# Performance work log

Hardware: AMD Instinct MI355X
Metric: run time of the kernel (lower is better)

## Reference

```python
import jax, jax.numpy as jnp
import numpy as np

HIDDEN = 2048
HEADS = 16
HEAD_DIM = HIDDEN // HEADS
BLOCK = 64
SEQ = 4096
NUM_BLOCKS = SEQ // BLOCK
N_LOCAL = 3
N_GLOBAL = 1
N_RANDOM = 1
SCALE = 1.0 / np.sqrt(HEAD_DIM)


def _sparse_mask(rand_idx):
    # rand_idx: [num_blocks, n_random] int -- random key-block per query-block row
    i = jnp.arange(NUM_BLOCKS)[:, None]
    j = jnp.arange(NUM_BLOCKS)[None, :]
    half = N_LOCAL // 2
    local = (j >= i - half) & (j <= i + half)
    glob = (j < N_GLOBAL) | (j >= NUM_BLOCKS - N_GLOBAL)
    rand = jnp.any(j[:, :, None] == rand_idx[:, None, :], axis=-1)
    blk = local | glob | rand                      # [nb, nb] bool
    full = jnp.repeat(jnp.repeat(blk, BLOCK, axis=0), BLOCK, axis=1)
    return full[:SEQ, :SEQ]                        # [S, S] bool


def setup_inputs() -> dict:
    key = jax.random.key(0)
    k1, k2, k3, k4, k5, k6 = jax.random.split(key, 6)
    s = 0.02
    return {
        "hidden_states": jax.random.normal(k1, (1, SEQ, HIDDEN), jnp.float32),
        "rand_idx": jax.random.randint(k2, (NUM_BLOCKS, N_RANDOM), 0, NUM_BLOCKS, jnp.int32),
        "Wq": jax.random.normal(k3, (HIDDEN, HIDDEN), jnp.float32) * s,
        "Wk": jax.random.normal(k4, (HIDDEN, HIDDEN), jnp.float32) * s,
        "Wv": jax.random.normal(k5, (HIDDEN, HIDDEN), jnp.float32) * s,
        "Wo": jax.random.normal(k6, (HIDDEN, HIDDEN), jnp.float32) * s,
    }


def reference(hidden_states, rand_idx, Wq, Wk, Wv, Wo):
    B, S, _ = hidden_states.shape
    # torch Linear: y = x @ W.T
    q = (hidden_states @ Wq.T).reshape(B, S, HEADS, HEAD_DIM).transpose(0, 2, 1, 3)
    k = (hidden_states @ Wk.T).reshape(B, S, HEADS, HEAD_DIM).transpose(0, 2, 1, 3)
    v = (hidden_states @ Wv.T).reshape(B, S, HEADS, HEAD_DIM).transpose(0, 2, 1, 3)
    scores = jnp.einsum("bhqd,bhkd->bhqk", q, k) * SCALE
    mask = _sparse_mask(rand_idx)                  # [S, S] bool
    scores = jnp.where(mask[None, None, :, :], scores, -jnp.inf)
    probs = jax.nn.softmax(scores, axis=-1)
    out = jnp.einsum("bhqk,bhkd->bhqd", probs, v)
    out = out.transpose(0, 2, 1, 3).reshape(B, S, HIDDEN)
    return out @ Wo.T
```

## Files before the change

kernel.cpp:

```cpp
#include <hip/hip_runtime.h>

typedef unsigned short u16;
typedef unsigned short u16x8 __attribute__((ext_vector_type(8)));
typedef __bf16 bf16x8 __attribute__((ext_vector_type(8)));
typedef float f32x4 __attribute__((ext_vector_type(4)));

#define SEQQ 4096
#define HID 2048
#define HD 128
#define NBLK 64
#define ATT_SCALE 0.08838834764831843f

__device__ __forceinline__ u16 f2bf(float f) {
    unsigned u = __float_as_uint(f);
    u += 0x7fffu + ((u >> 16) & 1u);
    return (u16)(u >> 16);
}

__device__ __forceinline__ void gload_lds16(const void* g, void* l) {
    __builtin_amdgcn_global_load_lds((const __attribute__((address_space(1))) void*)g,
                                     (__attribute__((address_space(3))) void*)l, 16, 0, 0);
}

__global__ __launch_bounds__(256) void cvt_bf16_k(const float* __restrict__ in,
                                                  u16* __restrict__ out, int n4) {
    int i = blockIdx.x * 256 + threadIdx.x;
    if (i < n4) {
        float4 v = ((const float4*)in)[i];
        ushort4 o;
        o.x = f2bf(v.x); o.y = f2bf(v.y); o.z = f2bf(v.z); o.w = f2bf(v.w);
        ((ushort4*)out)[i] = o;
    }
}

__global__ __launch_bounds__(256) void cvt4_k(const float* __restrict__ w0,
                                              const float* __restrict__ w1,
                                              const float* __restrict__ w2,
                                              const float* __restrict__ w3,
                                              u16* __restrict__ qkv,
                                              u16* __restrict__ wo) {
    const int y = blockIdx.y;
    const float* src = (y == 0) ? w0 : (y == 1) ? w1 : (y == 2) ? w2 : w3;
    u16* dst = (y < 3) ? (qkv + (size_t)y * 4194304) : wo;
    int i = blockIdx.x * 256 + threadIdx.x;
    float4 v = ((const float4*)src)[i];
    ushort4 o;
    o.x = f2bf(v.x); o.y = f2bf(v.y); o.z = f2bf(v.z); o.w = f2bf(v.w);
    ((ushort4*)dst)[i] = o;
}

#define QUAD(MH, AF, BF)                                                        \
    __builtin_amdgcn_s_setprio(1);                                              \
    _Pragma("unroll") for (int mi = 0; mi < 4; ++mi) {                          \
        _Pragma("unroll") for (int ni = 0; ni < 4; ++ni)                        \
            acc[(MH) * 4 + mi][ni] = __builtin_amdgcn_mfma_f32_16x16x32_bf16(   \
                (AF)[mi], (BF)[ni], acc[(MH) * 4 + mi][ni], 0, 0, 0);           \
    }                                                                           \
    __builtin_amdgcn_s_setprio(0);

template <int MODE>
__global__ __launch_bounds__(512, 2) void gemm256(const u16* __restrict__ A,
                                                  const u16* __restrict__ B,
                                                  void* __restrict__ C0,
                                                  u16* __restrict__ C1,
                                                  u16* __restrict__ C2,
                                                  int M, int N, int K) {
    __shared__ __align__(16) u16 As[2][2][4][256][8];
    __shared__ __align__(16) u16 Bs[2][2][4][256][8];
    const int t = threadIdx.x, w = t >> 6, l = t & 63;
    const int wm = w >> 2, wn = w & 3, ll = l & 15, lg = l >> 4;

    const int gx = gridDim.x, gy = gridDim.y;
    const int nwg = gx * gy;
    int lid = blockIdx.y * gx + blockIdx.x;
    int swz = (lid & 7) * (nwg >> 3) + (lid >> 3);
    const int mb = swz % gy, nb = swz / gy;

    const int c1 = t, c2 = t + 512;
    const u16* gA1 = A + (size_t)(mb * 256 + (c1 & 255)) * K + (c1 >> 8) * 8;
    const u16* gA2 = A + (size_t)(mb * 256 + (c2 & 255)) * K + (c2 >> 8) * 8;
    const u16* gB1 = B + (size_t)(nb * 256 + (c1 & 255)) * K + (c1 >> 8) * 8;
    const u16* gB2 = B + (size_t)(nb * 256 + (c2 & 255)) * K + (c2 >> 8) * 8;

    f32x4 acc[8][4] = {};

    auto stageA = [&](int buf, int kh, int kt) {
        gload_lds16(gA1 + kt * 64 + kh * 32, &As[buf][kh][c1 >> 8][c1 & 255][0]);
        gload_lds16(gA2 + kt * 64 + kh * 32, &As[buf][kh][c2 >> 8][c2 & 255][0]);
    };
    auto stageB = [&](int buf, int kh, int kt) {
        gload_lds16(gB1 + kt * 64 + kh * 32, &Bs[buf][kh][c1 >> 8][c1 & 255][0]);
        gload_lds16(gB2 + kt * 64 + kh * 32, &Bs[buf][kh][c2 >> 8][c2 & 255][0]);
    };
    auto fragsA = [&](int buf, int kh, int mh, bf16x8* af) {
#pragma unroll
        for (int mi = 0; mi < 4; ++mi)
            af[mi] = *(const bf16x8*)&As[buf][kh][lg][wm * 128 + mh * 64 + mi * 16 + ll][0];
    };
    auto fragsB = [&](int buf, int kh, bf16x8* bf) {
#pragma unroll
        for (int ni = 0; ni < 4; ++ni)
            bf[ni] = *(const bf16x8*)&Bs[buf][kh][lg][wn * 64 + ni * 16 + ll][0];
    };

    stageA(0, 0, 0); stageB(0, 0, 0); stageA(0, 1, 0); stageB(0, 1, 0);
    asm volatile("s_waitcnt vmcnt(4)" ::: "memory");
    asm volatile("s_barrier" ::: "memory");

    const int T = K >> 6;
    for (int kt = 0; kt < T; ++kt) {
        const int buf = kt & 1, nbuf = buf ^ 1;
        const bool last = (kt == T - 1);
        bf16x8 a0[4], a1[4], b0[4];
        fragsA(buf, 0, 0, a0); fragsB(buf, 0, b0);
        if (!last) stageA(nbuf, 0, kt + 1);
        asm volatile("s_barrier" ::: "memory");
        QUAD(0, a0, b0)
        asm volatile("s_barrier" ::: "memory");
        fragsA(buf, 0, 1, a1);
        if (!last) {
            stageB(nbuf, 0, kt + 1);
            asm volatile("s_waitcnt vmcnt(4)" ::: "memory");
        } else {
            asm volatile("s_waitcnt vmcnt(0)" ::: "memory");
        }
        asm volatile("s_barrier" ::: "memory");
        QUAD(1, a1, b0)
        asm volatile("s_barrier" ::: "memory");
        fragsA(buf, 1, 0, a0); fragsB(buf, 1, b0);
        if (!last) stageA(nbuf, 1, kt + 1);
        asm volatile("s_barrier" ::: "memory");
        QUAD(0, a0, b0)
        asm volatile("s_barrier" ::: "memory");
        fragsA(buf, 1, 1, a1);
        if (!last) {
            stageB(nbuf, 1, kt + 1);
            asm volatile("s_waitcnt vmcnt(4)" ::: "memory");
        }
        asm volatile("s_barrier" ::: "memory");
        QUAD(1, a1, b0)
        asm volatile("s_barrier" ::: "memory");
    }

    const int colb = nb * 256;
    u16* dstq = nullptr;
    int coff = 0;
    if (MODE == 1) {
        if (colb < 2048)      { dstq = (u16*)C0; coff = colb; }
        else if (colb < 4096) { dstq = C1; coff = colb - 2048; }
        else                  { dstq = C2; coff = colb - 4096; }
    }
#pragma unroll
    for (int mi = 0; mi < 8; ++mi)
#pragma unroll
        for (int ni = 0; ni < 4; ++ni) {
            f32x4 v = acc[mi][ni];
#pragma unroll
            for (int r = 0; r < 4; ++r) {
                int row = mb * 256 + wm * 128 + mi * 16 + lg * 4 + r;
                int col = wn * 64 + ni * 16 + ll;
                if (MODE == 0)
                    ((float*)C0)[(size_t)row * N + colb + col] = v[r];
                else
                    dstq[(size_t)row * 2048 + coff + col] = f2bf(v[r]);
            }
        }
}

__global__ __launch_bounds__(256) void transpose_k(const u16* __restrict__ in,
                                                   u16* __restrict__ out) {
    __shared__ __align__(16) u16 tl[64][64];
    const int s0 = blockIdx.x * 64, d0 = blockIdx.y * 64;
    const int t = threadIdx.x;
#pragma unroll
    for (int j = 0; j < 2; ++j) {
        int c = j * 256 + t;
        int sr = c >> 3, c8 = c & 7;
        u16x8 v = *(const u16x8*)&in[(size_t)(s0 + sr) * 2048 + d0 + c8 * 8];
        *(u16x8*)&tl[sr][(c8 ^ (sr >> 3)) * 8] = v;
    }
    __syncthreads();
#pragma unroll
    for (int j = 0; j < 2; ++j) {
        int c = j * 256 + t;
        int dr = c >> 3, sg = c & 7;
        u16x8 v;
#pragma unroll
        for (int i = 0; i < 8; ++i)
            v[i] = tl[sg * 8 + i][(((dr >> 3) ^ sg) * 8) + (dr & 7)];
        *(u16x8*)&out[(size_t)(d0 + dr) * 4096 + s0 + sg * 8] = v;
    }
}

__global__ __launch_bounds__(256) void sparse_attn(const u16* __restrict__ Q,
                                                   const u16* __restrict__ Kmat,
                                                   const u16* __restrict__ Vt,
                                                   const int* __restrict__ rnd,
                                                   u16* __restrict__ Out) {
    __shared__ __align__(16) u16 Ks[2][8192];
    __shared__ __align__(16) u16 Vs[2][8192];
    __shared__ __align__(16) char Plds[4 * 2048];

    const int qb = blockIdx.x, h = blockIdx.y;
    const int t = threadIdx.x, w = t >> 6, l = t & 63;
    const int lg = l >> 4, ll = l & 15;

    int blist[6];
    int nblk = 0;
    {
        int cands[6];
        cands[0] = qb - 1; cands[1] = qb; cands[2] = qb + 1;
        cands[3] = 0; cands[4] = NBLK - 1; cands[5] = rnd[qb];
        for (int c = 0; c < 6; ++c) {
            int b = cands[c];
            if (b < 0 || b >= NBLK) continue;
            bool dup = false;
            for (int j = 0; j < nblk; ++j) dup = dup || (blist[j] == b);
            if (!dup) blist[nblk++] = b;
        }
    }

    auto stage = [&](int buf, int kb) {
        const u16* kbase = Kmat + (size_t)(kb * 64) * HID + h * HD;
        const u16* vbase = Vt + (size_t)(h * HD) * SEQQ + kb * 64;
#pragma unroll
        for (int j = 0; j < 4; ++j) {
            int d = j * 256 + t;
            int kr = d >> 4, kc_ = (d & 15) ^ (kr & 7);
            gload_lds16(kbase + (size_t)kr * HID + kc_ * 8, &Ks[buf][d * 8]);
            int vr = d >> 3, vc = (d & 7) ^ (vr & 7);
            gload_lds16(vbase + (size_t)vr * SEQQ + vc * 8, &Vs[buf][d * 8]);
        }
    };

    bf16x8 qf[4];
    const int qrow = qb * 64 + w * 16 + ll;
#pragma unroll
    for (int kc = 0; kc < 4; ++kc)
        qf[kc] = *(const bf16x8*)&Q[(size_t)qrow * HID + h * HD + kc * 32 + lg * 8];

    f32x4 o[8];
#pragma unroll
    for (int dt = 0; dt < 8; ++dt) o[dt] = (f32x4){0.f, 0.f, 0.f, 0.f};
    float mrun[4], lrun[4];
#pragma unroll
    for (int r = 0; r < 4; ++r) { mrun[r] = -1e30f; lrun[r] = 0.f; }

    char* Pw = Plds + w * 2048;

    stage(0, blist[0]);
    int cur = 0;

    for (int bi = 0; bi < nblk; ++bi) {
        if (bi + 1 < nblk) {
            stage(cur ^ 1, blist[bi + 1]);
            asm volatile("s_waitcnt vmcnt(8)\n\ts_barrier" ::: "memory");
        } else {
            asm volatile("s_waitcnt vmcnt(0)\n\ts_barrier" ::: "memory");
        }

        f32x4 s[4];
#pragma unroll
        for (int ct = 0; ct < 4; ++ct) s[ct] = (f32x4){0.f, 0.f, 0.f, 0.f};
#pragma unroll
        for (int ct = 0; ct < 4; ++ct) {
            const int krow = ct * 16 + ll;
#pragma unroll
            for (int kc = 0; kc < 4; ++kc) {
                bf16x8 kf = *(const bf16x8*)&Ks[cur][krow * 128 +
                                                    (((kc * 4 + lg) ^ (krow & 7)) << 3)];
                s[ct] = __builtin_amdgcn_mfma_f32_16x16x32_bf16(qf[kc], kf, s[ct], 0, 0, 0);
            }
        }

        float rmax[4];
#pragma unroll
        for (int r = 0; r < 4; ++r) {
            s[0][r] *= ATT_SCALE; s[1][r] *= ATT_SCALE;
            s[2][r] *= ATT_SCALE; s[3][r] *= ATT_SCALE;
            rmax[r] = fmaxf(fmaxf(s[0][r], s[1][r]), fmaxf(s[2][r], s[3][r]));
        }
#pragma unroll
        for (int mk = 1; mk <= 8; mk <<= 1)
#pragma unroll
            for (int r = 0; r < 4; ++r)
                rmax[r] = fmaxf(rmax[r], __shfl_xor(rmax[r], mk));

        float scl[4], psum[4];
#pragma unroll
        for (int r = 0; r < 4; ++r) {
            float mn = fmaxf(mrun[r], rmax[r]);
            scl[r] = __expf(mrun[r] - mn);
            mrun[r] = mn;
            psum[r] = 0.f;
        }

#pragma unroll
        for (int ct = 0; ct < 4; ++ct)
#pragma unroll
            for (int r = 0; r < 4; ++r) {
                float e = __expf(s[ct][r] - mrun[r]);
                psum[r] += e;
                const int q = lg * 4 + r;
                const int kv = ct * 16 + ll;
                *(u16*)(Pw + q * 128 + ((kv * 2) ^ ((q & 7) << 4))) = f2bf(e);
            }
#pragma unroll
        for (int mk = 1; mk <= 8; mk <<= 1)
#pragma unroll
            for (int r = 0; r < 4; ++r)
                psum[r] += __shfl_xor(psum[r], mk);
#pragma unroll
        for (int r = 0; r < 4; ++r)
            lrun[r] = lrun[r] * scl[r] + psum[r];
#pragma unroll
        for (int dt = 0; dt < 8; ++dt)
#pragma unroll
            for (int r = 0; r < 4; ++r)
                o[dt][r] *= scl[r];

#pragma unroll
        for (int kc2 = 0; kc2 < 2; ++kc2) {
            bf16x8 pf = *(const bf16x8*)(Pw + ll * 128 +
                                         ((kc2 * 64 + lg * 16) ^ ((ll & 7) << 4)));
#pragma unroll
            for (int dt = 0; dt < 8; ++dt) {
                const int vrow = dt * 16 + ll;
                bf16x8 vf = *(const bf16x8*)&Vs[cur][vrow * 64 +
                                                     (((kc2 * 4 + lg) ^ (vrow & 7)) << 3)];
                o[dt] = __builtin_amdgcn_mfma_f32_16x16x32_bf16(pf, vf, o[dt], 0, 0, 0);
            }
        }

        asm volatile("s_barrier" ::: "memory");
        cur ^= 1;
    }

    float rl[4];
#pragma unroll
    for (int r = 0; r < 4; ++r) rl[r] = 1.f / lrun[r];
#pragma unroll
    for (int dt = 0; dt < 8; ++dt)
#pragma unroll
        for (int r = 0; r < 4; ++r) {
            int row = qb * 64 + w * 16 + lg * 4 + r;
            int col = h * HD + dt * 16 + ll;
            Out[(size_t)row * HID + col] = f2bf(o[dt][r] * rl[r]);
        }
}

extern "C" void kernel_launch(void* const* d_in, const int* in_sizes, int n_in,
                              void* d_out, int out_size, void* d_ws, size_t ws_size,
                              hipStream_t stream) {
    const float* hs = (const float*)d_in[0];
    const int* rnd = (const int*)d_in[1];
    const float* Wq = (const float*)d_in[2];
    const float* Wk = (const float*)d_in[3];
    const float* Wv = (const float*)d_in[4];
    const float* Wo = (const float*)d_in[5];
    float* out = (float*)d_out;

    char* ws = (char*)d_ws;
    u16* hs_b   = (u16*)(ws);
    u16* Wqkv_b = (u16*)(ws + 16777216);
    u16* Wo_b   = (u16*)(ws + 41943040);
    u16* Qb     = (u16*)(ws + 50331648);
    u16* Kb     = (u16*)(ws + 67108864);
    u16* Vtb    = (u16*)(ws + 83886080);
    u16* Ab     = (u16*)(ws + 100663296);

    cvt_bf16_k<<<dim3(8192), 256, 0, stream>>>(hs, hs_b, 8388608 / 4);
    cvt4_k<<<dim3(4096, 4), 256, 0, stream>>>(Wq, Wk, Wv, Wo, Wqkv_b, Wo_b);

    gemm256<1><<<dim3(24, 16), 512, 0, stream>>>(hs_b, Wqkv_b, Qb, Kb, Ab, 4096, 6144, 2048);

    transpose_k<<<dim3(64, 32), 256, 0, stream>>>(Ab, Vtb);

    sparse_attn<<<dim3(64, 16), 256, 0, stream>>>(Qb, Kb, Vtb, rnd, Ab);

    gemm256<0><<<dim3(8, 16), 512, 0, stream>>>(Ab, Wo_b, out, nullptr, nullptr, 4096, 2048, 2048);
}
```

Baseline: 477.0 us.

## Use 128x256 GEMM tiles with triple-buffered LDS and load attention V directly

```diff
diff --git a/kernel.cpp b/kernel.cpp
--- a/kernel.cpp
+++ b/kernel.cpp
@@ -49,97 +49,95 @@
     ((ushort4*)dst)[i] = o;
 }
 
-#define QUAD(MH, AF, BF)                                                        \
-    __builtin_amdgcn_s_setprio(1);                                              \
-    _Pragma("unroll") for (int mi = 0; mi < 4; ++mi) {                          \
-        _Pragma("unroll") for (int ni = 0; ni < 4; ++ni)                        \
-            acc[(MH) * 4 + mi][ni] = __builtin_amdgcn_mfma_f32_16x16x32_bf16(   \
-                (AF)[mi], (BF)[ni], acc[(MH) * 4 + mi][ni], 0, 0, 0);           \
-    }                                                                           \
-    __builtin_amdgcn_s_setprio(0);
-
 template <int MODE>
-__global__ __launch_bounds__(512, 2) void gemm256(const u16* __restrict__ A,
-                                                  const u16* __restrict__ B,
-                                                  void* __restrict__ C0,
-                                                  u16* __restrict__ C1,
-                                                  u16* __restrict__ C2,
-                                                  int M, int N, int K) {
-    __shared__ __align__(16) u16 As[2][2][4][256][8];
-    __shared__ __align__(16) u16 Bs[2][2][4][256][8];
+__global__ __launch_bounds__(512, 2) void gemm_p(const u16* __restrict__ A,
+                                                 const u16* __restrict__ B,
+                                                 void* __restrict__ C0,
+                                                 u16* __restrict__ C1,
+                                                 u16* __restrict__ C2,
+                                                 int M, int N, int K) {
+    __shared__ __align__(16) u16 As[3][2][4][128][8];
+    __shared__ __align__(16) u16 Bs[3][2][4][256][8];
     const int t = threadIdx.x, w = t >> 6, l = t & 63;
-    const int wm = w >> 2, wn = w & 3, ll = l & 15, lg = l >> 4;
+    const int ll = l & 15, lg = l >> 4;
+    const int wm = w >> 2, wn = w & 3;
 
     const int gx = gridDim.x, gy = gridDim.y;
-    const int nwg = gx * gy;
+    const int per = (gx * gy) >> 3;
     int lid = blockIdx.y * gx + blockIdx.x;
-    int swz = (lid & 7) * (nwg >> 3) + (lid >> 3);
-    const int mb = swz % gy, nb = swz / gy;
-
-    const int c1 = t, c2 = t + 512;
-    const u16* gA1 = A + (size_t)(mb * 256 + (c1 & 255)) * K + (c1 >> 8) * 8;
-    const u16* gA2 = A + (size_t)(mb * 256 + (c2 & 255)) * K + (c2 >> 8) * 8;
-    const u16* gB1 = B + (size_t)(nb * 256 + (c1 & 255)) * K + (c1 >> 8) * 8;
-    const u16* gB2 = B + (size_t)(nb * 256 + (c2 & 255)) * K + (c2 >> 8) * 8;
-
-    f32x4 acc[8][4] = {};
-
-    auto stageA = [&](int buf, int kh, int kt) {
-        gload_lds16(gA1 + kt * 64 + kh * 32, &As[buf][kh][c1 >> 8][c1 & 255][0]);
-        gload_lds16(gA2 + kt * 64 + kh * 32, &As[buf][kh][c2 >> 8][c2 & 255][0]);
+    int virt = (lid & 7) * per + (lid >> 3);
+    const int nb = virt % gx, mb = virt / gx;
+
+    f32x4 acc[4][4] = {};
+
+    const int akg = (t >> 7) & 3, arow = t & 127;
+    const int bkg = t >> 8, brow = t & 255;
+    const u16* gA = A + (size_t)(mb * 128 + arow) * K + akg * 8;
+    const u16* gB = B + (size_t)(nb * 256 + brow) * K;
+
+    auto stageA = [&](int sb, int kt) {
+        const u16* p = gA + kt * 64;
+        gload_lds16(p, &As[sb][0][akg][arow][0]);
+        gload_lds16(p + 32, &As[sb][1][akg][arow][0]);
     };
-    auto stageB = [&](int buf, int kh, int kt) {
-        gload_lds16(gB1 + kt * 64 + kh * 32, &Bs[buf][kh][c1 >> 8][c1 & 255][0]);
-        gload_lds16(gB2 + kt * 64 + kh * 32, &Bs[buf][kh][c2 >> 8][c2 & 255][0]);
+    auto stageB = [&](int sb, int kt) {
+        const u16* p = gB + kt * 64;
+        gload_lds16(p + bkg * 8,        &Bs[sb][0][bkg][brow][0]);
+        gload_lds16(p + (bkg + 2) * 8,  &Bs[sb][0][bkg + 2][brow][0]);
+        gload_lds16(p + 32 + bkg * 8,   &Bs[sb][1][bkg][brow][0]);
+        gload_lds16(p + 32 + (bkg + 2) * 8, &Bs[sb][1][bkg + 2][brow][0]);
     };
-    auto fragsA = [&](int buf, int kh, int mh, bf16x8* af) {
+
+    stageA(0, 0); stageB(0, 0); stageA(1, 1); stageB(1, 1);
+    asm volatile("s_waitcnt vmcnt(6)" ::: "memory");
+    __builtin_amdgcn_s_barrier();
+
+    const int T = K >> 6;
+    int buf = 0;
+    for (int kt = 0; kt < T; ++kt) {
+        const int sb = (buf + 2 >= 3) ? buf - 1 : buf + 2;
+        const bool st = (kt + 2) < T;
+        bf16x8 af[4], bfr[4];
 #pragma unroll
         for (int mi = 0; mi < 4; ++mi)
-            af[mi] = *(const bf16x8*)&As[buf][kh][lg][wm * 128 + mh * 64 + mi * 16 + ll][0];
-    };
-    auto fragsB = [&](int buf, int kh, bf16x8* bf) {
+            af[mi] = *(const bf16x8*)&As[buf][0][lg][wm * 64 + mi * 16 + ll][0];
 #pragma unroll
         for (int ni = 0; ni < 4; ++ni)
-            bf[ni] = *(const bf16x8*)&Bs[buf][kh][lg][wn * 64 + ni * 16 + ll][0];
-    };
-
-    stageA(0, 0, 0); stageB(0, 0, 0); stageA(0, 1, 0); stageB(0, 1, 0);
-    asm volatile("s_waitcnt vmcnt(4)" ::: "memory");
-    asm volatile("s_barrier" ::: "memory");
-
-    const int T = K >> 6;
-    for (int kt = 0; kt < T; ++kt) {
-        const int buf = kt & 1, nbuf = buf ^ 1;
-        const bool last = (kt == T - 1);
-        bf16x8 a0[4], a1[4], b0[4];
-        fragsA(buf, 0, 0, a0); fragsB(buf, 0, b0);
-        if (!last) stageA(nbuf, 0, kt + 1);
-        asm volatile("s_barrier" ::: "memory");
-        QUAD(0, a0, b0)
-        asm volatile("s_barrier" ::: "memory");
-        fragsA(buf, 0, 1, a1);
-        if (!last) {
-            stageB(nbuf, 0, kt + 1);
-            asm volatile("s_waitcnt vmcnt(4)" ::: "memory");
+            bfr[ni] = *(const bf16x8*)&Bs[buf][0][lg][wn * 64 + ni * 16 + ll][0];
+        if (st) stageA(sb, kt + 2);
+        __builtin_amdgcn_s_barrier();
+        __builtin_amdgcn_s_setprio(1);
+#pragma unroll
+        for (int mi = 0; mi < 4; ++mi)
+#pragma unroll
+            for (int ni = 0; ni < 4; ++ni)
+                acc[mi][ni] = __builtin_amdgcn_mfma_f32_16x16x32_bf16(af[mi], bfr[ni],
+                                                                      acc[mi][ni], 0, 0, 0);
+        __builtin_amdgcn_s_setprio(0);
+        bf16x8 ag[4], bgr[4];
+#pragma unroll
+        for (int mi = 0; mi < 4; ++mi)
+            ag[mi] = *(const bf16x8*)&As[buf][1][lg][wm * 64 + mi * 16 + ll][0];
+#pragma unroll
+        for (int ni = 0; ni < 4; ++ni)
+            bgr[ni] = *(const bf16x8*)&Bs[buf][1][lg][wn * 64 + ni * 16 + ll][0];
+        if (st) {
+            stageB(sb, kt + 2);
+            asm volatile("s_waitcnt vmcnt(6)" ::: "memory");
         } else {
             asm volatile("s_waitcnt vmcnt(0)" ::: "memory");
         }
-        asm volatile("s_barrier" ::: "memory");
-        QUAD(1, a1, b0)
-        asm volatile("s_barrier" ::: "memory");
-        fragsA(buf, 1, 0, a0); fragsB(buf, 1, b0);
-        if (!last) stageA(nbuf, 1, kt + 1);
-        asm volatile("s_barrier" ::: "memory");
-        QUAD(0, a0, b0)
-        asm volatile("s_barrier" ::: "memory");
-        fragsA(buf, 1, 1, a1);
-        if (!last) {
-            stageB(nbuf, 1, kt + 1);
-            asm volatile("s_waitcnt vmcnt(4)" ::: "memory");
-        }
-        asm volatile("s_barrier" ::: "memory");
-        QUAD(1, a1, b0)
-        asm volatile("s_barrier" ::: "memory");
+        __builtin_amdgcn_s_barrier();
+        __builtin_amdgcn_s_setprio(1);
+#pragma unroll
+        for (int mi = 0; mi < 4; ++mi)
+#pragma unroll
+            for (int ni = 0; ni < 4; ++ni)
+                acc[mi][ni] = __builtin_amdgcn_mfma_f32_16x16x32_bf16(ag[mi], bgr[ni],
+                                                                      acc[mi][ni], 0, 0, 0);
+        __builtin_amdgcn_s_setprio(0);
+        __builtin_amdgcn_s_barrier();
+        buf = (buf + 1 == 3) ? 0 : buf + 1;
     }
 
     const int colb = nb * 256;
@@ -151,13 +149,13 @@
         else                  { dstq = C2; coff = colb - 4096; }
     }
 #pragma unroll
-    for (int mi = 0; mi < 8; ++mi)
+    for (int mi = 0; mi < 4; ++mi)
 #pragma unroll
         for (int ni = 0; ni < 4; ++ni) {
             f32x4 v = acc[mi][ni];
 #pragma unroll
             for (int r = 0; r < 4; ++r) {
-                int row = mb * 256 + wm * 128 + mi * 16 + lg * 4 + r;
+                int row = mb * 128 + wm * 64 + mi * 16 + lg * 4 + r;
                 int col = wn * 64 + ni * 16 + ll;
                 if (MODE == 0)
                     ((float*)C0)[(size_t)row * N + colb + col] = v[r];
@@ -197,8 +195,7 @@
                                                    const u16* __restrict__ Vt,
                                                    const int* __restrict__ rnd,
                                                    u16* __restrict__ Out) {
-    __shared__ __align__(16) u16 Ks[2][8192];
-    __shared__ __align__(16) u16 Vs[2][8192];
+    __shared__ __align__(16) u16 Ks[3][8192];
     __shared__ __align__(16) char Plds[4 * 2048];
 
     const int qb = blockIdx.x, h = blockIdx.y;
@@ -220,16 +217,13 @@
         }
     }
 
-    auto stage = [&](int buf, int kb) {
+    auto stageK = [&](int sb, int kb) {
         const u16* kbase = Kmat + (size_t)(kb * 64) * HID + h * HD;
-        const u16* vbase = Vt + (size_t)(h * HD) * SEQQ + kb * 64;
 #pragma unroll
         for (int j = 0; j < 4; ++j) {
             int d = j * 256 + t;
             int kr = d >> 4, kc_ = (d & 15) ^ (kr & 7);
-            gload_lds16(kbase + (size_t)kr * HID + kc_ * 8, &Ks[buf][d * 8]);
-            int vr = d >> 3, vc = (d & 7) ^ (vr & 7);
-            gload_lds16(vbase + (size_t)vr * SEQQ + vc * 8, &Vs[buf][d * 8]);
+            gload_lds16(kbase + (size_t)kr * HID + kc_ * 8, &Ks[sb][d * 8]);
         }
     };
 
@@ -248,16 +242,31 @@
 
     char* Pw = Plds + w * 2048;
 
-    stage(0, blist[0]);
-    int cur = 0;
+    stageK(0, blist[0]);
+    if (nblk > 1) stageK(1, blist[1]);
+    int buf = 0;
 
     for (int bi = 0; bi < nblk; ++bi) {
-        if (bi + 1 < nblk) {
-            stage(cur ^ 1, blist[bi + 1]);
-            asm volatile("s_waitcnt vmcnt(8)\n\ts_barrier" ::: "memory");
+        const int kb = blist[bi];
+        const bool st = (bi + 2) < nblk;
+        const int sb = (buf + 2 >= 3) ? buf - 1 : buf + 2;
+        if (st) {
+            stageK(sb, blist[bi + 2]);
+            asm volatile("s_waitcnt vmcnt(8)" ::: "memory");
+        } else if (bi + 1 < nblk) {
+            asm volatile("s_waitcnt vmcnt(4)" ::: "memory");
         } else {
-            asm volatile("s_waitcnt vmcnt(0)\n\ts_barrier" ::: "memory");
-        }
+            asm volatile("s_waitcnt vmcnt(0)" ::: "memory");
+        }
+        __builtin_amdgcn_s_barrier();
+
+        bf16x8 vf[16];
+#pragma unroll
+        for (int kc2 = 0; kc2 < 2; ++kc2)
+#pragma unroll
+            for (int dt = 0; dt < 8; ++dt)
+                vf[kc2 * 8 + dt] = *(const bf16x8*)&Vt[(size_t)(h * HD + dt * 16 + ll) * SEQQ +
+                                                       kb * 64 + kc2 * 32 + lg * 8];
 
         f32x4 s[4];
 #pragma unroll
@@ -267,7 +276,7 @@
             const int krow = ct * 16 + ll;
 #pragma unroll
             for (int kc = 0; kc < 4; ++kc) {
-                bf16x8 kf = *(const bf16x8*)&Ks[cur][krow * 128 +
+                bf16x8 kf = *(const bf16x8*)&Ks[buf][krow * 128 +
                                                     (((kc * 4 + lg) ^ (krow & 7)) << 3)];
                 s[ct] = __builtin_amdgcn_mfma_f32_16x16x32_bf16(qf[kc], kf, s[ct], 0, 0, 0);
             }
@@ -324,16 +333,13 @@
             bf16x8 pf = *(const bf16x8*)(Pw + ll * 128 +
                                          ((kc2 * 64 + lg * 16) ^ ((ll & 7) << 4)));
 #pragma unroll
-            for (int dt = 0; dt < 8; ++dt) {
-                const int vrow = dt * 16 + ll;
-                bf16x8 vf = *(const bf16x8*)&Vs[cur][vrow * 64 +
-                                                     (((kc2 * 4 + lg) ^ (vrow & 7)) << 3)];
-                o[dt] = __builtin_amdgcn_mfma_f32_16x16x32_bf16(pf, vf, o[dt], 0, 0, 0);
-            }
-        }
-
-        asm volatile("s_barrier" ::: "memory");
-        cur ^= 1;
+            for (int dt = 0; dt < 8; ++dt)
+                o[dt] = __builtin_amdgcn_mfma_f32_16x16x32_bf16(pf, vf[kc2 * 8 + dt],
+                                                                o[dt], 0, 0, 0);
+        }
+
+        __builtin_amdgcn_s_barrier();
+        buf = (buf + 1 == 3) ? 0 : buf + 1;
     }
 
     float rl[4];
@@ -372,11 +378,11 @@
     cvt_bf16_k<<<dim3(8192), 256, 0, stream>>>(hs, hs_b, 8388608 / 4);
     cvt4_k<<<dim3(4096, 4), 256, 0, stream>>>(Wq, Wk, Wv, Wo, Wqkv_b, Wo_b);
 
-    gemm256<1><<<dim3(24, 16), 512, 0, stream>>>(hs_b, Wqkv_b, Qb, Kb, Ab, 4096, 6144, 2048);
+    gemm_p<1><<<dim3(24, 32), 512, 0, stream>>>(hs_b, Wqkv_b, Qb, Kb, Ab, 4096, 6144, 2048);
 
     transpose_k<<<dim3(64, 32), 256, 0, stream>>>(Ab, Vtb);
 
     sparse_attn<<<dim3(64, 16), 256, 0, stream>>>(Qb, Kb, Vtb, rnd, Ab);
 
-    gemm256<0><<<dim3(8, 16), 512, 0, stream>>>(Ab, Wo_b, out, nullptr, nullptr, 4096, 2048, 2048);
-}
+    gemm_p<0><<<dim3(8, 32), 512, 0, stream>>>(Ab, Wo_b, out, nullptr, nullptr, 4096, 2048, 2048);
+}
```

New measurement: 437.5 us. -8.3%, faster.
